# Kernel tuning notes

Measured on AMD Instinct MI355X. Metric: run time of the kernel, lower is better.

The kernel has to match this reference:

```python
import jax, jax.numpy as jnp
import numpy as np

# SMPL 24-joint kinematic tree (parent of joint j); root has parent -1.
PARENTS = [-1, 0, 0, 0, 1, 2, 3, 4, 5, 6, 7, 8, 9, 9, 9, 12, 13, 14, 16, 17, 18, 19, 20, 21]
N_JOINTS = len(PARENTS)  # 24


def setup_inputs() -> dict:
    key = jax.random.key(0)
    k1, k2 = jax.random.split(key)
    N = 262144
    joint_angles = jax.random.normal(k1, (N, N_JOINTS * 9), dtype=jnp.float32)
    offsets = jax.random.normal(k2, (N_JOINTS, 3), dtype=jnp.float32)
    return {"joint_angles": joint_angles, "offsets": offsets}


def reference(joint_angles, offsets):
    # joint_angles: (N, n_joints*9) -> (N, n_joints, 3, 3)
    N = joint_angles.shape[0]
    ang = joint_angles.reshape(N, N_JOINTS, 3, 3)
    # no_root=True: force the root rotation to identity
    ang = ang.at[:, 0].set(jnp.eye(3, dtype=ang.dtype))

    rotations = [ang[:, 0]]                              # (N,3,3)
    positions = [jnp.zeros((N, 3), dtype=ang.dtype)]     # (N,3)
    # Sequential tree recurrence over fixed small joint count (right-mult path,
    # left_mult=False): pos_j = R_parent @ offset_j + pos_parent;
    # R_j = R_parent @ A_j.
    for j in range(1, N_JOINTS):
        p = PARENTS[j]
        pos = jnp.einsum('nij,j->ni', rotations[p], offsets[j]) + positions[p]
        rot = jnp.einsum('nij,njk->nik', rotations[p], ang[:, j])
        positions.append(pos)
        rotations.append(rot)

    return jnp.stack(positions, axis=1)  # (N, n_joints, 3)
```

## Files before the change

### kernel.cpp

```cpp
#include <hip/hip_runtime.h>

namespace {

typedef float v4f __attribute__((ext_vector_type(4)));

struct M3 { float a[9]; };
struct V3 { float x, y, z; };

__device__ __forceinline__ V3 mulv_add(const M3& R, V3 o, V3 p) {
    V3 r;
    r.x = fmaf(R.a[0], o.x, fmaf(R.a[1], o.y, fmaf(R.a[2], o.z, p.x)));
    r.y = fmaf(R.a[3], o.x, fmaf(R.a[4], o.y, fmaf(R.a[5], o.z, p.y)));
    r.z = fmaf(R.a[6], o.x, fmaf(R.a[7], o.y, fmaf(R.a[8], o.z, p.z)));
    return r;
}

__device__ __forceinline__ M3 mulm(const M3& R, const M3& A) {
    M3 D;
#pragma unroll
    for (int i = 0; i < 3; ++i) {
#pragma unroll
        for (int k = 0; k < 3; ++k) {
            D.a[i*3+k] = fmaf(R.a[i*3+0], A.a[0*3+k],
                         fmaf(R.a[i*3+1], A.a[1*3+k],
                              R.a[i*3+2] * A.a[2*3+k]));
        }
    }
    return D;
}

template <int REL>
__device__ __forceinline__ float getf(const float4* s) {
    constexpr int Q = REL >> 2;
    constexpr int C = REL & 3;
    if constexpr (C == 0) return s[Q].x;
    else if constexpr (C == 1) return s[Q].y;
    else if constexpr (C == 2) return s[Q].z;
    else return s[Q].w;
}

template <int J, int BASE>
__device__ __forceinline__ M3 loadA(const float4* s) {
    constexpr int K = 9 * J - BASE;
    M3 A;
    A.a[0] = getf<K+0>(s); A.a[1] = getf<K+1>(s); A.a[2] = getf<K+2>(s);
    A.a[3] = getf<K+3>(s); A.a[4] = getf<K+4>(s); A.a[5] = getf<K+5>(s);
    A.a[6] = getf<K+6>(s); A.a[7] = getf<K+7>(s); A.a[8] = getf<K+8>(s);
    return A;
}

__device__ __forceinline__ V3 loadOff(const float* __restrict__ off, int j) {
    V3 o; o.x = off[3*j+0]; o.y = off[3*j+1]; o.z = off[3*j+2]; return o;
}

__device__ __forceinline__ void gload16(const float4* src, float4* lds_base) {
    __builtin_amdgcn_global_load_lds(
        (const __attribute__((address_space(1))) void*)src,
        (__attribute__((address_space(3))) void*)lds_base, 16, 0, 0);
}

#define OBP(J, P) do { ob[3*(J)+0] = (P).x; ob[3*(J)+1] = (P).y; ob[3*(J)+2] = (P).z; } while (0)

__global__ __launch_bounds__(64, 2)
void fk_kernel(const float* __restrict__ ja, const float* __restrict__ off,
               float* __restrict__ out) {
    __shared__ __align__(16) float4 lds[1344];
    float4* A1 = lds;
    float4* stage = lds;

    const int l = threadIdx.x;
    const size_t blockBase = (size_t)blockIdx.x * 64;
    const float4* g = reinterpret_cast<const float4*>(ja) + blockBase * 54;
    const float4* row = g + (size_t)l * 54;

    float4 s2[7];
#pragma unroll
    for (int c = 0; c < 7; ++c) s2[c] = row[27 + c];
    float4 s3[14];
#pragma unroll
    for (int c = 0; c < 14; ++c) s3[c] = row[36 + c];

#pragma unroll
    for (int k = 0; k < 21; ++k) {
        int p = k * 64 + l;
        int s = p / 21, j = p - s * 21;
        gload16(g + s * 54 + 2 + j, A1 + k * 64);
    }

    float ob[72];
    ob[0] = 0.f; ob[1] = 0.f; ob[2] = 0.f;

    asm volatile("s_waitcnt vmcnt(0)" ::: "memory");

    float4 s1[21];
    {
        const float4* r1 = A1 + l * 21;
#pragma unroll
        for (int c = 0; c < 21; ++c) s1[c] = r1[c];
    }
    constexpr int B1 = 8, B2 = 108, B3 = 144;

    V3 p1 = loadOff(off, 1), p2 = loadOff(off, 2), p3 = loadOff(off, 3);
    OBP(1, p1); OBP(2, p2); OBP(3, p3);
    M3 R1 = loadA<1, B1>(s1);
    M3 R2 = loadA<2, B1>(s1);
    M3 R3 = loadA<3, B1>(s1);

    V3 p4 = mulv_add(R1, loadOff(off, 4), p1);  M3 R4 = mulm(R1, loadA<4, B1>(s1));  OBP(4, p4);
    V3 p5 = mulv_add(R2, loadOff(off, 5), p2);  M3 R5 = mulm(R2, loadA<5, B1>(s1));  OBP(5, p5);
    V3 p6 = mulv_add(R3, loadOff(off, 6), p3);  M3 R6 = mulm(R3, loadA<6, B1>(s1));  OBP(6, p6);
    V3 p7 = mulv_add(R4, loadOff(off, 7), p4);  M3 R7 = mulm(R4, loadA<7, B1>(s1));  OBP(7, p7);
    V3 p8 = mulv_add(R5, loadOff(off, 8), p5);  M3 R8 = mulm(R5, loadA<8, B1>(s1));  OBP(8, p8);
    V3 p9 = mulv_add(R6, loadOff(off, 9), p6);  M3 R9 = mulm(R6, loadA<9, B1>(s1));  OBP(9, p9);

    V3 p10 = mulv_add(R7, loadOff(off, 10), p7);  OBP(10, p10);
    V3 p11 = mulv_add(R8, loadOff(off, 11), p8);  OBP(11, p11);

    V3 p12 = mulv_add(R9, loadOff(off, 12), p9);  M3 R12 = mulm(R9, loadA<12, B2>(s2));  OBP(12, p12);
    V3 p13 = mulv_add(R9, loadOff(off, 13), p9);  M3 R13 = mulm(R9, loadA<13, B2>(s2));  OBP(13, p13);
    V3 p14 = mulv_add(R9, loadOff(off, 14), p9);  M3 R14 = mulm(R9, loadA<14, B2>(s2));  OBP(14, p14);
    V3 p15 = mulv_add(R12, loadOff(off, 15), p12);  OBP(15, p15);

    V3 p16 = mulv_add(R13, loadOff(off, 16), p13);  M3 R16 = mulm(R13, loadA<16, B3>(s3));  OBP(16, p16);
    V3 p17 = mulv_add(R14, loadOff(off, 17), p14);  M3 R17 = mulm(R14, loadA<17, B3>(s3));  OBP(17, p17);
    V3 p18 = mulv_add(R16, loadOff(off, 18), p16);  M3 R18 = mulm(R16, loadA<18, B3>(s3));  OBP(18, p18);
    V3 p19 = mulv_add(R17, loadOff(off, 19), p17);  M3 R19 = mulm(R17, loadA<19, B3>(s3));  OBP(19, p19);
    V3 p20 = mulv_add(R18, loadOff(off, 20), p18);  M3 R20 = mulm(R18, loadA<20, B3>(s3));  OBP(20, p20);
    V3 p21 = mulv_add(R19, loadOff(off, 21), p19);  M3 R21 = mulm(R19, loadA<21, B3>(s3));  OBP(21, p21);

    V3 p22 = mulv_add(R20, loadOff(off, 22), p20);  OBP(22, p22);
    V3 p23 = mulv_add(R21, loadOff(off, 23), p21);  OBP(23, p23);

    asm volatile("" ::: "memory");
#pragma unroll
    for (int r = 0; r < 18; ++r) {
        float4 v;
        v.x = ob[4*r+0]; v.y = ob[4*r+1]; v.z = ob[4*r+2]; v.w = ob[4*r+3];
        stage[r * 65 + l] = v;
    }

    v4f* o4 = reinterpret_cast<v4f*>(out);
    const size_t base4 = blockBase * 18;
#pragma unroll
    for (int i = 0; i < 18; ++i) {
        int e4 = i * 64 + l;
        int s  = e4 / 18;
        int r  = e4 - s * 18;
        float4 v = stage[r * 65 + s];
        v4f vv; vv.x = v.x; vv.y = v.y; vv.z = v.z; vv.w = v.w;
        __builtin_nontemporal_store(vv, &o4[base4 + e4]);
    }
}

}

extern "C" void kernel_launch(void* const* d_in, const int* in_sizes, int n_in,
                              void* d_out, int out_size, void* d_ws, size_t ws_size,
                              hipStream_t stream) {
    const float* ja  = (const float*)d_in[0];
    const float* off = (const float*)d_in[1];
    float* out = (float*)d_out;

    int N = in_sizes[0] / 216;
    int grid = N / 64;
    hipLaunchKernelGGL(fk_kernel, dim3(grid), dim3(64), 0, stream, ja, off, out);
}
```

Baseline: 51.46 us.

## Process eight chunks per block with double-buffered LDS prefetch pipeline

Each 64-thread block now handles eight 64-row chunks instead of one. Loads for the next chunk go into a second LDS buffer and register set while the current chunk is computed and stored, with manual vmcnt waits between stages. The grid shrinks eightfold and launch bounds drop to one block per SIMD. This trades far fewer resident waves for software overlap, which risks hiding memory latency worse on a bandwidth-bound kernel.

```diff
diff --git a/kernel.cpp b/kernel.cpp
--- a/kernel.cpp
+++ b/kernel.cpp
@@ -59,46 +59,38 @@
         (__attribute__((address_space(3))) void*)lds_base, 16, 0, 0);
 }
 
-#define OBP(J, P) do { ob[3*(J)+0] = (P).x; ob[3*(J)+1] = (P).y; ob[3*(J)+2] = (P).z; } while (0)
-
-__global__ __launch_bounds__(64, 2)
-void fk_kernel(const float* __restrict__ ja, const float* __restrict__ off,
-               float* __restrict__ out) {
-    __shared__ __align__(16) float4 lds[1344];
-    float4* A1 = lds;
-    float4* stage = lds;
-
-    const int l = threadIdx.x;
-    const size_t blockBase = (size_t)blockIdx.x * 64;
-    const float4* g = reinterpret_cast<const float4*>(ja) + blockBase * 54;
-    const float4* row = g + (size_t)l * 54;
-
-    float4 s2[7];
+__device__ __forceinline__ void issue_loads(const float4* gc, int l,
+                                            float4* buf,
+                                            float4 (&s2)[7], float4 (&s3)[14]) {
+    const float4* row = gc + (size_t)l * 54;
 #pragma unroll
     for (int c = 0; c < 7; ++c) s2[c] = row[27 + c];
-    float4 s3[14];
 #pragma unroll
     for (int c = 0; c < 14; ++c) s3[c] = row[36 + c];
-
 #pragma unroll
     for (int k = 0; k < 21; ++k) {
         int p = k * 64 + l;
         int s = p / 21, j = p - s * 21;
-        gload16(g + s * 54 + 2 + j, A1 + k * 64);
+        gload16(gc + s * 54 + 2 + j, buf + k * 64);
     }
+}
 
-    float ob[72];
-    ob[0] = 0.f; ob[1] = 0.f; ob[2] = 0.f;
+#define OBP(J, P) do { ob[3*(J)+0] = (P).x; ob[3*(J)+1] = (P).y; ob[3*(J)+2] = (P).z; } while (0)
 
-    asm volatile("s_waitcnt vmcnt(0)" ::: "memory");
+__device__ __forceinline__ void compute_store(
+    int l, float4* buf, const float4 (&s2)[7], const float4 (&s3)[14],
+    const float* __restrict__ off, v4f* oc) {
 
     float4 s1[21];
     {
-        const float4* r1 = A1 + l * 21;
+        const float4* r1 = buf + l * 21;
 #pragma unroll
         for (int c = 0; c < 21; ++c) s1[c] = r1[c];
     }
     constexpr int B1 = 8, B2 = 108, B3 = 144;
+
+    float ob[72];
+    ob[0] = 0.f; ob[1] = 0.f; ob[2] = 0.f;
 
     V3 p1 = loadOff(off, 1), p2 = loadOff(off, 2), p3 = loadOff(off, 3);
     OBP(1, p1); OBP(2, p2); OBP(3, p3);
@@ -131,6 +123,7 @@
     V3 p22 = mulv_add(R20, loadOff(off, 22), p20);  OBP(22, p22);
     V3 p23 = mulv_add(R21, loadOff(off, 23), p21);  OBP(23, p23);
 
+    float4* stage = buf;
     asm volatile("" ::: "memory");
 #pragma unroll
     for (int r = 0; r < 18; ++r) {
@@ -139,8 +132,6 @@
         stage[r * 65 + l] = v;
     }
 
-    v4f* o4 = reinterpret_cast<v4f*>(out);
-    const size_t base4 = blockBase * 18;
 #pragma unroll
     for (int i = 0; i < 18; ++i) {
         int e4 = i * 64 + l;
@@ -148,7 +139,44 @@
         int r  = e4 - s * 18;
         float4 v = stage[r * 65 + s];
         v4f vv; vv.x = v.x; vv.y = v.y; vv.z = v.z; vv.w = v.w;
-        __builtin_nontemporal_store(vv, &o4[base4 + e4]);
+        __builtin_nontemporal_store(vv, &oc[e4]);
+    }
+}
+
+__global__ __launch_bounds__(64, 1)
+void fk_kernel(const float* __restrict__ ja, const float* __restrict__ off,
+               float* __restrict__ out) {
+    __shared__ __align__(16) float4 lds[2688];
+    float4* buf0 = lds;
+    float4* buf1 = lds + 1344;
+
+    const int l = threadIdx.x;
+    const int b = blockIdx.x;
+    const float4* ja4 = reinterpret_cast<const float4*>(ja);
+    v4f* o4 = reinterpret_cast<v4f*>(out);
+
+    auto gc = [&](int c) { return ja4 + (size_t)(b * 8 + c) * 3456; };
+    auto oc = [&](int c) { return o4  + (size_t)(b * 8 + c) * 1152; };
+
+    float4 s2A[7], s3A[14], s2B[7], s3B[14];
+
+    issue_loads(gc(0), l, buf0, s2A, s3A);
+
+#pragma unroll 1
+    for (int it = 0; it < 4; ++it) {
+        const int c0 = 2 * it, c1 = 2 * it + 1;
+
+        issue_loads(gc(c1), l, buf1, s2B, s3B);
+        asm volatile("s_waitcnt vmcnt(42)" ::: "memory");
+        compute_store(l, buf0, s2A, s3A, off, oc(c0));
+
+        if (it < 3) {
+            issue_loads(gc(c0 + 2), l, buf0, s2A, s3A);
+            asm volatile("s_waitcnt vmcnt(42)" ::: "memory");
+        } else {
+            asm volatile("s_waitcnt vmcnt(0)" ::: "memory");
+        }
+        compute_store(l, buf1, s2B, s3B, off, oc(c1));
     }
 }
 
@@ -162,6 +190,6 @@
     float* out = (float*)d_out;
 
     int N = in_sizes[0] / 216;
-    int grid = N / 64;
+    int grid = N / 512;
     hipLaunchKernelGGL(fk_kernel, dim3(grid), dim3(64), 0, stream, ja, off, out);
 }
```

New measurement: 57.40 us. 11.6% more time.
